# Optimization experiments

Hardware: AMD Instinct MI355X
Metric: run time of the kernel (lower is better)

The kernel has to match this reference:

```python
import jax, jax.numpy as jnp
import numpy as np

BN_EPS = 1e-5

def setup_inputs() -> dict:
    key = jax.random.key(0)
    ks = jax.random.split(key, 13)
    bs, ch, hei, wei = 4, 32, 32, 128  # n_features = wei = 128, ch = n_features//4
    nf = wei
    def p(k, shape, s=0.05):
        return jax.random.normal(k, shape, dtype=jnp.float32) * s
    return {
        "head": jax.random.normal(ks[0], (bs, ch, hei, wei), dtype=jnp.float32),
        "tail": jax.random.normal(ks[1], (bs, ch, hei, wei), dtype=jnp.float32),
        "R_q": p(ks[2], (nf, nf)), "R_k": p(ks[3], (nf, nf)),
        "R_v": p(ks[4], (nf, nf)), "R_W": p(ks[5], (nf, nf)),
        "F_q": p(ks[6], (nf, nf)), "F_k": p(ks[7], (nf, nf)),
        "F_v": p(ks[8], (nf, nf)), "F_W": p(ks[9], (nf, nf)),
        "conv_w": p(ks[10], (2, 2 * ch, 1, 1)),
        "conv_b": jnp.zeros((2,), jnp.float32),
        "bn_w": jnp.ones((2,), jnp.float32),
        "bn_b": jnp.zeros((2,), jnp.float32),
        "bn_mean": jnp.zeros((2,), jnp.float32),
        "bn_var": jnp.ones((2,), jnp.float32),
        "flag": 1,
    }

def _affinity(head, tail, conv_w, conv_b, bn_w, bn_b, bn_mean, bn_var):
    # 1x1 conv -> eval-mode BatchNorm2d -> ReLU -> softmax over channel dim
    x = jnp.concatenate([head, tail], axis=1)                       # [b,2c,h,w]
    a = jnp.einsum('bchw,oc->bohw', x, conv_w[:, :, 0, 0]) + conv_b[None, :, None, None]
    scale = (bn_w / jnp.sqrt(bn_var + BN_EPS))[None, :, None, None]
    a = (a - bn_mean[None, :, None, None]) * scale + bn_b[None, :, None, None]
    a = jax.nn.relu(a)
    return jax.nn.softmax(a, axis=1)                                # torch legacy dim=1 for 4D

def reference(head, tail, R_q, R_k, R_v, R_W, F_q, F_k, F_v, F_W,
              conv_w, conv_b, bn_w, bn_b, bn_mean, bn_var, flag):
    bs, ch, hei, wei = head.shape
    L = hei * wei
    ic = ch  # inter_channels == ch by construction
    aff = _affinity(head, tail, conv_w, conv_b, bn_w, bn_b, bn_mean, bn_var)
    if flag:
        alpha = aff[:, 0].reshape(bs, L, 1)                          # broadcast over last axis
        q = (head @ R_q).reshape(bs, ic, L).transpose(0, 2, 1)       # [b,L,ic]
        t_k = (tail @ F_k).reshape(bs, ic, L).transpose(0, 2, 1)     # [b,L,ic]
        t_v = (tail @ F_v).reshape(bs, ic, L)                        # [b,ic,L]
        f_t = t_k @ t_v                                              # [b,L,L]
        h_k = (head @ R_k).reshape(bs, ic, L).transpose(0, 2, 1)
        h_v = (head @ R_v).reshape(bs, ic, L)
        f_h = h_k @ h_v                                              # [b,L,L]
        att = jax.nn.softmax(alpha * f_t + f_h, axis=-1)
        y = (att @ q).transpose(0, 2, 1).reshape(bs, ic, hei, wei)
        return y @ R_W + head
    else:
        alpha = aff[:, 1].reshape(bs, L, 1)
        q = (tail @ F_q).reshape(bs, ic, L).transpose(0, 2, 1)
        h_k = (head @ R_k).reshape(bs, ic, L).transpose(0, 2, 1)
        h_v = (head @ R_v).reshape(bs, ic, L)
        f_h = h_k @ h_v
        t_k = (tail @ F_k).reshape(bs, ic, L).transpose(0, 2, 1)
        t_v = (tail @ F_v).reshape(bs, ic, L)
        f_t = t_k @ t_v
        att = jax.nn.softmax(alpha * f_h + f_t, axis=-1)
        y = (att @ q).transpose(0, 2, 1).reshape(bs, ic, hei, wei)
        return y @ F_W + tail
```

## Files before the change

kernel.cpp:

```cpp
#include <hip/hip_runtime.h>
#include <hip/hip_bf16.h>
#include <stdint.h>

typedef unsigned short u16;
typedef unsigned int u32;
typedef __attribute__((ext_vector_type(8))) short short8;
typedef __attribute__((ext_vector_type(4))) short short4_t;
typedef __attribute__((ext_vector_type(4))) float f32x4;

#define MFMA16(A,B,C) __builtin_amdgcn_mfma_f32_16x16x32_bf16((A),(B),(C),0,0,0)
#define L2E 1.4426950408889634f

__device__ __forceinline__ u16 f2bf(float f) {
  u32 x = __float_as_uint(f);
  u32 r = x + 0x7fffu + ((x >> 16) & 1u);
  return (u16)(r >> 16);
}
__device__ __forceinline__ float bf2f(short v) {
  return __uint_as_float((u32)(u16)v << 16);
}
__device__ __forceinline__ u32 pack_bf2(float a, float b) {
  __hip_bfloat162 h = __float22bfloat162_rn(make_float2(a, b));
  u32 u; __builtin_memcpy(&u, &h, 4); return u;
}
__device__ __forceinline__ short8 mk_frag(u32 w0, u32 w1, u32 w2, u32 w3) {
  union { u32 u[4]; short8 s; } cv;
  cv.u[0] = w0; cv.u[1] = w1; cv.u[2] = w2; cv.u[3] = w3;
  return cv.s;
}
__device__ __forceinline__ float vmax4(f32x4 v) {
  return fmaxf(fmaxf(v[0], v[1]), fmaxf(v[2], v[3]));
}
__device__ __forceinline__ float vsum4(f32x4 v) {
  return (v[0] + v[1]) + (v[2] + v[3]);
}

#if __has_builtin(__builtin_amdgcn_permlane16_swap) && __has_builtin(__builtin_amdgcn_permlane32_swap)
__device__ __forceinline__ float quad_max16(float x) {
  u32 xu = __float_as_uint(x);
  auto a = __builtin_amdgcn_permlane16_swap(xu, xu, false, false);
  float m = fmaxf(__uint_as_float(a[0]), __uint_as_float(a[1]));
  u32 mu = __float_as_uint(m);
  auto b = __builtin_amdgcn_permlane32_swap(mu, mu, false, false);
  return fmaxf(__uint_as_float(b[0]), __uint_as_float(b[1]));
}
__device__ __forceinline__ float quad_sum16(float x) {
  u32 xu = __float_as_uint(x);
  auto a = __builtin_amdgcn_permlane16_swap(xu, xu, false, false);
  float m = __uint_as_float(a[0]) + __uint_as_float(a[1]);
  u32 mu = __float_as_uint(m);
  auto b = __builtin_amdgcn_permlane32_swap(mu, mu, false, false);
  return __uint_as_float(b[0]) + __uint_as_float(b[1]);
}
#else
__device__ __forceinline__ float quad_max16(float x) {
  x = fmaxf(x, __shfl_xor(x, 16, 64));
  return fmaxf(x, __shfl_xor(x, 32, 64));
}
__device__ __forceinline__ float quad_sum16(float x) {
  x += __shfl_xor(x, 16, 64);
  return x + __shfl_xor(x, 32, 64);
}
#endif

__global__ void kprep(const float* R_q, const float* R_k, const float* R_v,
                      const float* R_W, const float* F_q, const float* F_k,
                      const float* F_v, const float* F_W, const int* flagp,
                      u16* matT)
{
  int flag = *flagp;
  const float* S;
  int m = blockIdx.x;
  if (flag) {
    const float* s[6] = {R_q, R_k, R_v, F_k, F_v, R_W}; S = s[m];
  } else {
    const float* s[6] = {F_q, F_k, F_v, R_k, R_v, F_W}; S = s[m];
  }
  u16* dst = matT + m * 16384;
  int base = blockIdx.y * 2048;
  for (int idx = base + threadIdx.x; idx < base + 2048; idx += blockDim.x) {
    int k = idx >> 7, n = idx & 127;
    dst[n * 128 + k] = f2bf(S[idx]);
  }
}

__global__ __launch_bounds__(256) void kproj(const float* __restrict__ head,
    const float* __restrict__ tail, const u16* __restrict__ matT,
    const float* __restrict__ conv_w, const float* __restrict__ conv_b,
    const float* __restrict__ bn_w, const float* __restrict__ bn_b,
    const float* __restrict__ bn_mean, const float* __restrict__ bn_var,
    u16* __restrict__ qT, u16* __restrict__ KQ,
    u16* __restrict__ Vc, const int* __restrict__ flagp)
{
  __shared__ u16 lds_t[128][34];
  __shared__ float s_alpha[128];
  const int flag = *flagp;
  const float* X1 = flag ? head : tail;
  const float* X2 = flag ? tail : head;
  const int bh = blockIdx.x, g = blockIdx.y;
  const int b = bh >> 5, h = bh & 31;
  const float* src = (g < 3) ? X1 : X2;
  const u16* Bm = matT + g * 16384;
  const int tid = threadIdx.x, lane = tid & 63, wid = tid >> 6;
  const int lrow = lane & 15, lg = lane >> 4;
  const int rt = wid & 1, cbase = (wid >> 1) * 64;

  if (g == 3) {
    if (tid < 128) {
      int w = tid;
      const float* hp = head + ((size_t)b * 1024 + h) * 128 + w;
      const float* tp = tail + ((size_t)b * 1024 + h) * 128 + w;
      float a0 = 0.f, a1 = 0.f;
      for (int c = 0; c < 32; ++c) {
        float xh = hp[c * 4096];
        float xt = tp[c * 4096];
        a0 += xh * conv_w[c]      + xt * conv_w[32 + c];
        a1 += xh * conv_w[64 + c] + xt * conv_w[96 + c];
      }
      const float eps = 1e-5f;
      a0 += conv_b[0]; a1 += conv_b[1];
      a0 = (a0 - bn_mean[0]) * (bn_w[0] * rsqrtf(bn_var[0] + eps)) + bn_b[0];
      a1 = (a1 - bn_mean[1]) * (bn_w[1] * rsqrtf(bn_var[1] + eps)) + bn_b[1];
      a0 = fmaxf(a0, 0.f); a1 = fmaxf(a1, 0.f);
      float asel = flag ? a0 : a1, aoth = flag ? a1 : a0;
      s_alpha[w] = 1.f / (1.f + __expf(aoth - asel));
    }
    __syncthreads();
  }

  f32x4 acc[4] = {};
  const float* Arow = src + (((size_t)b * 32 + rt * 16 + lrow) * 32 + h) * 128;
  #pragma unroll
  for (int k0 = 0; k0 < 128; k0 += 32) {
    const float* ap = Arow + k0 + lg * 8;
    float4 f0 = *reinterpret_cast<const float4*>(ap);
    float4 f1 = *reinterpret_cast<const float4*>(ap + 4);
    short8 af = mk_frag(pack_bf2(f0.x, f0.y), pack_bf2(f0.z, f0.w),
                        pack_bf2(f1.x, f1.y), pack_bf2(f1.z, f1.w));
    #pragma unroll
    for (int cc = 0; cc < 4; ++cc) {
      short8 bf = *reinterpret_cast<const short8*>(
          Bm + (cbase + cc * 16 + lrow) * 128 + k0 + lg * 8);
      acc[cc] = MFMA16(af, bf, acc[cc]);
    }
  }
  #pragma unroll
  for (int cc = 0; cc < 4; ++cc) {
    int n = cbase + cc * 16 + lrow;
    float asc = (g == 1) ? L2E : 1.f;
    if (g == 3) asc = s_alpha[n] * L2E;
    #pragma unroll
    for (int rr = 0; rr < 4; ++rr) {
      int c = rt * 16 + lg * 4 + rr;
      lds_t[n][c] = f2bf(acc[cc][rr] * asc);
    }
  }
  __syncthreads();
  if (g == 0) {
    int c = tid >> 3, w0 = (tid & 7) * 16;
    int tw[8];
    #pragma unroll
    for (int i2 = 0; i2 < 8; ++i2)
      tw[i2] = (int)lds_t[w0 + 2 * i2][c] | ((int)lds_t[w0 + 2 * i2 + 1][c] << 16);
    int4* dst = reinterpret_cast<int4*>(qT + ((size_t)b * 32 + c) * 4096 + h * 128 + w0);
    dst[0] = make_int4(tw[0], tw[1], tw[2], tw[3]);
    dst[1] = make_int4(tw[4], tw[5], tw[6], tw[7]);
  } else if (tid < 128) {
    int w = tid;
    int tw[16];
    #pragma unroll
    for (int i2 = 0; i2 < 16; ++i2)
      tw[i2] = (int)lds_t[w][2 * i2] | ((int)lds_t[w][2 * i2 + 1] << 16);
    u16* base = (g == 2 || g == 4) ? Vc : KQ;
    int coff = (g >= 3) ? 32 : 0;
    int4* dst = reinterpret_cast<int4*>(base + ((size_t)b * 4096 + h * 128 + w) * 64 + coff);
    dst[0] = make_int4(tw[0],  tw[1],  tw[2],  tw[3]);
    dst[1] = make_int4(tw[4],  tw[5],  tw[6],  tw[7]);
    dst[2] = make_int4(tw[8],  tw[9],  tw[10], tw[11]);
    dst[3] = make_int4(tw[12], tw[13], tw[14], tw[15]);
  }
}

__global__ __launch_bounds__(256, 6) void kattn(const u16* __restrict__ qT,
    const u16* __restrict__ KQ, const u16* __restrict__ Vc,
    u16* __restrict__ pO, float* __restrict__ pm, float* __restrict__ pl)
{
  __shared__ __align__(16) char lds_v[2][8192];
  __shared__ __align__(16) char lds_q[2][4096];
  const int b = blockIdx.y;
  const int i0 = blockIdx.x * 64;
  const int sp = blockIdx.z;
  const int jbase = sp * 512;
  const int tid = threadIdx.x, lane = tid & 63, wid = tid >> 6;
  const int lrow = lane & 15, lg = lane >> 4;

  const u16* KQb = KQ + (size_t)b * 4096 * 64;
  const u16* Vb  = Vc + (size_t)b * 4096 * 64;
  const u16* qTb = qT + (size_t)b * 32 * 4096;

  short8 bkq[2];
  {
    int r = i0 + wid * 16 + lrow;
    #pragma unroll
    for (int kc = 0; kc < 2; ++kc)
      bkq[kc] = *reinterpret_cast<const short8*>(KQb + (size_t)r * 64 + kc * 32 + lg * 8);
  }

  const int sr = tid >> 3, sx = (tid & 7) * 16;
  const int pr = (((sr >> 2) & 3) << 3) + (((sr >> 4) & 1) << 2) + (sr & 3);

  #pragma unroll
  for (int q = 0; q < 2; ++q) {
    int r = sr + q * 32, gr = pr + q * 32;
    int4 v = *reinterpret_cast<const int4*>(
        reinterpret_cast<const char*>(Vb + (size_t)(jbase + gr) * 64) + sx);
    *reinterpret_cast<int4*>(lds_v[0] + r * 128 + (sx ^ ((r & 7) << 4))) = v;
  }
  {
    int4 qv = *reinterpret_cast<const int4*>(
        qTb + (size_t)sr * 4096 + jbase + (tid & 7) * 8);
    *reinterpret_cast<int4*>(lds_q[0] + sr * 128 + (sx ^ ((sr & 7) << 4))) = qv;
  }
  __syncthreads();

  float m_run = -1e30f, l_run = 0.f;
  f32x4 accO[2] = {};
  int4 stgV[2], stgQ;

  for (int t = 0; t < 8; ++t) {
    const int buf = t & 1;
    if (t < 7) {
      const u16* Vn = Vb + (size_t)(jbase + (t + 1) * 64) * 64;
      #pragma unroll
      for (int q = 0; q < 2; ++q) {
        int gr = pr + q * 32;
        stgV[q] = *reinterpret_cast<const int4*>(
            reinterpret_cast<const char*>(Vn + (size_t)gr * 64) + sx);
      }
      stgQ = *reinterpret_cast<const int4*>(
          qTb + (size_t)sr * 4096 + jbase + (t + 1) * 64 + (tid & 7) * 8);
    }
    f32x4 st[4];
    __builtin_amdgcn_s_setprio(1);
    #pragma unroll
    for (int sub = 0; sub < 4; ++sub) {
      f32x4 a = {};
      #pragma unroll
      for (int kc = 0; kc < 2; ++kc) {
        int r = sub * 16 + lrow;
        int xs = kc * 64 + lg * 16;
        short8 av = *reinterpret_cast<const short8*>(
            lds_v[buf] + r * 128 + (xs ^ ((r & 7) << 4)));
        a = MFMA16(av, bkq[kc], a);
      }
      st[sub] = a;
    }
    __builtin_amdgcn_s_setprio(0);
    short8 aq[2][2];
    #pragma unroll
    for (int w = 0; w < 2; ++w)
      #pragma unroll
      for (int ct = 0; ct < 2; ++ct) {
        int r = ct * 16 + lrow;
        int xs = w * 64 + lg * 16;
        aq[w][ct] = *reinterpret_cast<const short8*>(
            lds_q[buf] + r * 128 + (xs ^ ((r & 7) << 4)));
      }
    float tm = fmaxf(fmaxf(vmax4(st[0]), vmax4(st[1])),
                     fmaxf(vmax4(st[2]), vmax4(st[3])));
    tm = quad_max16(tm);
    if (!__all((int)(tm <= m_run + 8.f))) {
      float m_new = fmaxf(m_run, tm);
      float scale = exp2f(m_run - m_new);
      l_run *= scale;
      #pragma unroll
      for (int ct = 0; ct < 2; ++ct)
        #pragma unroll
        for (int rr = 0; rr < 4; ++rr) accO[ct][rr] *= scale;
      m_run = m_new;
    }
    #pragma unroll
    for (int sub = 0; sub < 4; ++sub)
      #pragma unroll
      for (int rr = 0; rr < 4; ++rr)
        st[sub][rr] = exp2f(st[sub][rr] - m_run);
    float ps = (vsum4(st[0]) + vsum4(st[1])) + (vsum4(st[2]) + vsum4(st[3]));
    l_run += quad_sum16(ps);

    __builtin_amdgcn_s_setprio(1);
    #pragma unroll
    for (int w = 0; w < 2; ++w) {
      short8 bp = mk_frag(pack_bf2(st[2 * w][0],     st[2 * w][1]),
                          pack_bf2(st[2 * w][2],     st[2 * w][3]),
                          pack_bf2(st[2 * w + 1][0], st[2 * w + 1][1]),
                          pack_bf2(st[2 * w + 1][2], st[2 * w + 1][3]));
      #pragma unroll
      for (int ct = 0; ct < 2; ++ct)
        accO[ct] = MFMA16(aq[w][ct], bp, accO[ct]);
    }
    __builtin_amdgcn_s_setprio(0);

    if (t < 7) {
      #pragma unroll
      for (int q = 0; q < 2; ++q) {
        int r = sr + q * 32;
        *reinterpret_cast<int4*>(lds_v[buf ^ 1] + r * 128 + (sx ^ ((r & 7) << 4))) = stgV[q];
      }
      *reinterpret_cast<int4*>(lds_q[buf ^ 1] + sr * 128 + (sx ^ ((sr & 7) << 4))) = stgQ;
      __syncthreads();
    }
  }

  const int i = i0 + wid * 16 + lrow;
  u16* pOb = pO + (size_t)((b * 8 + sp) * 32) * 4096;
  #pragma unroll
  for (int ct = 0; ct < 2; ++ct)
    #pragma unroll
    for (int rr = 0; rr < 4; ++rr)
      pOb[(size_t)(ct * 16 + lg * 4 + rr) * 4096 + i] = f2bf(accO[ct][rr]);
  if (lg == 0) {
    pm[(b * 8 + sp) * 4096 + i] = m_run;
    pl[(b * 8 + sp) * 4096 + i] = l_run;
  }
}

__global__ __launch_bounds__(256) void kout(const u16* __restrict__ pO,
    const float* __restrict__ pm, const float* __restrict__ pl,
    const u16* __restrict__ matT, const float* __restrict__ head,
    const float* __restrict__ tail, const int* __restrict__ flagp,
    float* __restrict__ out)
{
  __shared__ u16 ylds[32][136];
  const int flag = *flagp;
  const float* X1 = flag ? head : tail;
  const u16* Bm = matT + 5 * 16384;
  const int tid = threadIdx.x;
  const int b = blockIdx.x >> 5, c = blockIdx.x & 31;
  const int rbase = blockIdx.x * 32;
  const int ioff = tid * 16;

  #pragma unroll
  for (int iq = 0; iq < 4; ++iq) {
    float4 msp[8];
    #pragma unroll
    for (int sp = 0; sp < 8; ++sp)
      msp[sp] = *reinterpret_cast<const float4*>(
          pm + (size_t)((b * 8 + sp) * 4096) + ioff + iq * 4);
    float4 M4 = msp[0];
    #pragma unroll
    for (int sp = 1; sp < 8; ++sp) {
      M4.x = fmaxf(M4.x, msp[sp].x); M4.y = fmaxf(M4.y, msp[sp].y);
      M4.z = fmaxf(M4.z, msp[sp].z); M4.w = fmaxf(M4.w, msp[sp].w);
    }
    float4 L4 = {0.f, 0.f, 0.f, 0.f}, y4 = {0.f, 0.f, 0.f, 0.f};
    #pragma unroll
    for (int sp = 0; sp < 8; ++sp) {
      float4 w4;
      w4.x = exp2f(msp[sp].x - M4.x); w4.y = exp2f(msp[sp].y - M4.y);
      w4.z = exp2f(msp[sp].z - M4.z); w4.w = exp2f(msp[sp].w - M4.w);
      float4 l4 = *reinterpret_cast<const float4*>(
          pl + (size_t)((b * 8 + sp) * 4096) + ioff + iq * 4);
      L4.x += w4.x * l4.x; L4.y += w4.y * l4.y;
      L4.z += w4.z * l4.z; L4.w += w4.w * l4.w;
      short4_t o4 = *reinterpret_cast<const short4_t*>(
          pO + (size_t)(((b * 8 + sp) * 32 + c)) * 4096 + ioff + iq * 4);
      y4.x += w4.x * bf2f(o4[0]); y4.y += w4.y * bf2f(o4[1]);
      y4.z += w4.z * bf2f(o4[2]); y4.w += w4.w * bf2f(o4[3]);
    }
    y4.x /= L4.x; y4.y /= L4.y; y4.z /= L4.z; y4.w /= L4.w;
    uint2 pk2;
    pk2.x = pack_bf2(y4.x, y4.y);
    pk2.y = pack_bf2(y4.z, y4.w);
    *reinterpret_cast<uint2*>(&ylds[tid >> 3][(tid & 7) * 16 + iq * 4]) = pk2;
  }
  __syncthreads();

  const int lane = tid & 63, wid = tid >> 6;
  const int lrow = lane & 15, lg = lane >> 4;
  const int rg = (wid & 1) * 16, cg = (wid >> 1) * 64;
  f32x4 acc[4] = {};
  #pragma unroll
  for (int k0 = 0; k0 < 128; k0 += 32) {
    short8 af = *reinterpret_cast<const short8*>(&ylds[rg + lrow][k0 + lg * 8]);
    #pragma unroll
    for (int cc = 0; cc < 4; ++cc) {
      short8 bf = *reinterpret_cast<const short8*>(
          Bm + (size_t)(cg + cc * 16 + lrow) * 128 + k0 + lg * 8);
      acc[cc] = MFMA16(af, bf, acc[cc]);
    }
  }
  #pragma unroll
  for (int cc = 0; cc < 4; ++cc)
    #pragma unroll
    for (int rr = 0; rr < 4; ++rr) {
      int row = rbase + rg + lg * 4 + rr;
      int col = cg + cc * 16 + lrow;
      size_t idx = (size_t)row * 128 + col;
      out[idx] = acc[cc][rr] + X1[idx];
    }
}

extern "C" void kernel_launch(void* const* d_in, const int* in_sizes, int n_in,
                              void* d_out, int out_size, void* d_ws, size_t ws_size,
                              hipStream_t stream)
{
  const float* head    = (const float*)d_in[0];
  const float* tail    = (const float*)d_in[1];
  const float* R_q     = (const float*)d_in[2];
  const float* R_k     = (const float*)d_in[3];
  const float* R_v     = (const float*)d_in[4];
  const float* R_W     = (const float*)d_in[5];
  const float* F_q     = (const float*)d_in[6];
  const float* F_k     = (const float*)d_in[7];
  const float* F_v     = (const float*)d_in[8];
  const float* F_W     = (const float*)d_in[9];
  const float* conv_w  = (const float*)d_in[10];
  const float* conv_b  = (const float*)d_in[11];
  const float* bn_w    = (const float*)d_in[12];
  const float* bn_b    = (const float*)d_in[13];
  const float* bn_mean = (const float*)d_in[14];
  const float* bn_var  = (const float*)d_in[15];
  const int*   flagp   = (const int*)d_in[16];
  float* out = (float*)d_out;

  char* ws = (char*)d_ws;
  u16*   matT = (u16*)(ws);
  u16*   qT   = (u16*)(ws + 262144);
  u16*   KQ   = (u16*)(ws + 1310720);
  u16*   Vc   = (u16*)(ws + 3407872);
  u16*   pO   = (u16*)(ws + 6553600);
  float* pm   = (float*)(ws + 14942208);
  float* pl   = (float*)(ws + 15466496);

  kprep <<<dim3(6, 8), 256, 0, stream>>>(R_q, R_k, R_v, R_W, F_q, F_k, F_v, F_W, flagp, matT);
  kproj <<<dim3(128, 5), 256, 0, stream>>>(head, tail, matT, conv_w, conv_b,
                                           bn_w, bn_b, bn_mean, bn_var,
                                           qT, KQ, Vc, flagp);
  kattn <<<dim3(64, 4, 8), 256, 0, stream>>>(qT, KQ, Vc, pO, pm, pl);
  kout  <<<128, 256, 0, stream>>>(pO, pm, pl, matT, head, tail, flagp, out);
}
```

Baseline: 66.28 us.

## Double split-K count in attention, preload all tiles, add separate merge kernel

```diff
diff --git a/kernel.cpp b/kernel.cpp
--- a/kernel.cpp
+++ b/kernel.cpp
@@ -181,16 +181,16 @@
   }
 }
 
-__global__ __launch_bounds__(256, 6) void kattn(const u16* __restrict__ qT,
+__global__ __launch_bounds__(256, 3) void kattn(const u16* __restrict__ qT,
     const u16* __restrict__ KQ, const u16* __restrict__ Vc,
     u16* __restrict__ pO, float* __restrict__ pm, float* __restrict__ pl)
 {
-  __shared__ __align__(16) char lds_v[2][8192];
-  __shared__ __align__(16) char lds_q[2][4096];
+  __shared__ __align__(16) char lds_v[4][8192];
+  __shared__ __align__(16) char lds_q[4][4096];
   const int b = blockIdx.y;
   const int i0 = blockIdx.x * 64;
   const int sp = blockIdx.z;
-  const int jbase = sp * 512;
+  const int jbase = sp * 256;
   const int tid = threadIdx.x, lane = tid & 63, wid = tid >> 6;
   const int lrow = lane & 15, lg = lane >> 4;
 
@@ -208,38 +208,26 @@
 
   const int sr = tid >> 3, sx = (tid & 7) * 16;
   const int pr = (((sr >> 2) & 3) << 3) + (((sr >> 4) & 1) << 2) + (sr & 3);
-
-  #pragma unroll
-  for (int q = 0; q < 2; ++q) {
-    int r = sr + q * 32, gr = pr + q * 32;
-    int4 v = *reinterpret_cast<const int4*>(
-        reinterpret_cast<const char*>(Vb + (size_t)(jbase + gr) * 64) + sx);
-    *reinterpret_cast<int4*>(lds_v[0] + r * 128 + (sx ^ ((r & 7) << 4))) = v;
-  }
-  {
+  #pragma unroll
+  for (int t = 0; t < 4; ++t) {
+    #pragma unroll
+    for (int q = 0; q < 2; ++q) {
+      int r = sr + q * 32, gr = pr + q * 32;
+      int4 v = *reinterpret_cast<const int4*>(
+          reinterpret_cast<const char*>(Vb + (size_t)(jbase + t * 64 + gr) * 64) + sx);
+      *reinterpret_cast<int4*>(lds_v[t] + r * 128 + (sx ^ ((r & 7) << 4))) = v;
+    }
     int4 qv = *reinterpret_cast<const int4*>(
-        qTb + (size_t)sr * 4096 + jbase + (tid & 7) * 8);
-    *reinterpret_cast<int4*>(lds_q[0] + sr * 128 + (sx ^ ((sr & 7) << 4))) = qv;
+        qTb + (size_t)sr * 4096 + jbase + t * 64 + (tid & 7) * 8);
+    *reinterpret_cast<int4*>(lds_q[t] + sr * 128 + (sx ^ ((sr & 7) << 4))) = qv;
   }
   __syncthreads();
 
   float m_run = -1e30f, l_run = 0.f;
   f32x4 accO[2] = {};
-  int4 stgV[2], stgQ;
-
-  for (int t = 0; t < 8; ++t) {
-    const int buf = t & 1;
-    if (t < 7) {
-      const u16* Vn = Vb + (size_t)(jbase + (t + 1) * 64) * 64;
-      #pragma unroll
-      for (int q = 0; q < 2; ++q) {
-        int gr = pr + q * 32;
-        stgV[q] = *reinterpret_cast<const int4*>(
-            reinterpret_cast<const char*>(Vn + (size_t)gr * 64) + sx);
-      }
-      stgQ = *reinterpret_cast<const int4*>(
-          qTb + (size_t)sr * 4096 + jbase + (t + 1) * 64 + (tid & 7) * 8);
-    }
+
+  #pragma unroll
+  for (int t = 0; t < 4; ++t) {
     f32x4 st[4];
     __builtin_amdgcn_s_setprio(1);
     #pragma unroll
@@ -250,7 +238,7 @@
         int r = sub * 16 + lrow;
         int xs = kc * 64 + lg * 16;
         short8 av = *reinterpret_cast<const short8*>(
-            lds_v[buf] + r * 128 + (xs ^ ((r & 7) << 4)));
+            lds_v[t] + r * 128 + (xs ^ ((r & 7) << 4)));
         a = MFMA16(av, bkq[kc], a);
       }
       st[sub] = a;
@@ -264,7 +252,7 @@
         int r = ct * 16 + lrow;
         int xs = w * 64 + lg * 16;
         aq[w][ct] = *reinterpret_cast<const short8*>(
-            lds_q[buf] + r * 128 + (xs ^ ((r & 7) << 4)));
+            lds_q[t] + r * 128 + (xs ^ ((r & 7) << 4)));
       }
     float tm = fmaxf(fmaxf(vmax4(st[0]), vmax4(st[1])),
                      fmaxf(vmax4(st[2]), vmax4(st[3])));
@@ -299,36 +287,48 @@
         accO[ct] = MFMA16(aq[w][ct], bp, accO[ct]);
     }
     __builtin_amdgcn_s_setprio(0);
-
-    if (t < 7) {
-      #pragma unroll
-      for (int q = 0; q < 2; ++q) {
-        int r = sr + q * 32;
-        *reinterpret_cast<int4*>(lds_v[buf ^ 1] + r * 128 + (sx ^ ((r & 7) << 4))) = stgV[q];
-      }
-      *reinterpret_cast<int4*>(lds_q[buf ^ 1] + sr * 128 + (sx ^ ((sr & 7) << 4))) = stgQ;
-      __syncthreads();
-    }
   }
 
   const int i = i0 + wid * 16 + lrow;
-  u16* pOb = pO + (size_t)((b * 8 + sp) * 32) * 4096;
+  u16* pOb = pO + (size_t)((b * 16 + sp) * 32) * 4096;
   #pragma unroll
   for (int ct = 0; ct < 2; ++ct)
     #pragma unroll
     for (int rr = 0; rr < 4; ++rr)
       pOb[(size_t)(ct * 16 + lg * 4 + rr) * 4096 + i] = f2bf(accO[ct][rr]);
   if (lg == 0) {
-    pm[(b * 8 + sp) * 4096 + i] = m_run;
-    pl[(b * 8 + sp) * 4096 + i] = l_run;
-  }
+    pm[(b * 16 + sp) * 4096 + i] = m_run;
+    pl[(b * 16 + sp) * 4096 + i] = l_run;
+  }
+}
+
+__global__ __launch_bounds__(256) void kmerge(const float* __restrict__ pm,
+    const float* __restrict__ pl, float* __restrict__ wm)
+{
+  const int b = blockIdx.y;
+  const int i = blockIdx.x * 256 + threadIdx.x;
+  float m[16], M = -1e30f;
+  #pragma unroll
+  for (int sp = 0; sp < 16; ++sp) {
+    m[sp] = pm[(b * 16 + sp) * 4096 + i];
+    M = fmaxf(M, m[sp]);
+  }
+  float L = 0.f;
+  #pragma unroll
+  for (int sp = 0; sp < 16; ++sp) {
+    m[sp] = exp2f(m[sp] - M);
+    L += m[sp] * pl[(b * 16 + sp) * 4096 + i];
+  }
+  float inv = 1.f / L;
+  #pragma unroll
+  for (int sp = 0; sp < 16; ++sp)
+    wm[(b * 16 + sp) * 4096 + i] = m[sp] * inv;
 }
 
 __global__ __launch_bounds__(256) void kout(const u16* __restrict__ pO,
-    const float* __restrict__ pm, const float* __restrict__ pl,
-    const u16* __restrict__ matT, const float* __restrict__ head,
-    const float* __restrict__ tail, const int* __restrict__ flagp,
-    float* __restrict__ out)
+    const float* __restrict__ wm, const u16* __restrict__ matT,
+    const float* __restrict__ head, const float* __restrict__ tail,
+    const int* __restrict__ flagp, float* __restrict__ out)
 {
   __shared__ u16 ylds[32][136];
   const int flag = *flagp;
@@ -341,33 +341,16 @@
 
   #pragma unroll
   for (int iq = 0; iq < 4; ++iq) {
-    float4 msp[8];
-    #pragma unroll
-    for (int sp = 0; sp < 8; ++sp)
-      msp[sp] = *reinterpret_cast<const float4*>(
-          pm + (size_t)((b * 8 + sp) * 4096) + ioff + iq * 4);
-    float4 M4 = msp[0];
-    #pragma unroll
-    for (int sp = 1; sp < 8; ++sp) {
-      M4.x = fmaxf(M4.x, msp[sp].x); M4.y = fmaxf(M4.y, msp[sp].y);
-      M4.z = fmaxf(M4.z, msp[sp].z); M4.w = fmaxf(M4.w, msp[sp].w);
-    }
-    float4 L4 = {0.f, 0.f, 0.f, 0.f}, y4 = {0.f, 0.f, 0.f, 0.f};
-    #pragma unroll
-    for (int sp = 0; sp < 8; ++sp) {
-      float4 w4;
-      w4.x = exp2f(msp[sp].x - M4.x); w4.y = exp2f(msp[sp].y - M4.y);
-      w4.z = exp2f(msp[sp].z - M4.z); w4.w = exp2f(msp[sp].w - M4.w);
-      float4 l4 = *reinterpret_cast<const float4*>(
-          pl + (size_t)((b * 8 + sp) * 4096) + ioff + iq * 4);
-      L4.x += w4.x * l4.x; L4.y += w4.y * l4.y;
-      L4.z += w4.z * l4.z; L4.w += w4.w * l4.w;
+    float4 y4 = {0.f, 0.f, 0.f, 0.f};
+    #pragma unroll
+    for (int sp = 0; sp < 16; ++sp) {
+      float4 w4 = *reinterpret_cast<const float4*>(
+          wm + (size_t)((b * 16 + sp) * 4096) + ioff + iq * 4);
       short4_t o4 = *reinterpret_cast<const short4_t*>(
-          pO + (size_t)(((b * 8 + sp) * 32 + c)) * 4096 + ioff + iq * 4);
+          pO + (size_t)(((b * 16 + sp) * 32 + c)) * 4096 + ioff + iq * 4);
       y4.x += w4.x * bf2f(o4[0]); y4.y += w4.y * bf2f(o4[1]);
       y4.z += w4.z * bf2f(o4[2]); y4.w += w4.w * bf2f(o4[3]);
     }
-    y4.x /= L4.x; y4.y /= L4.y; y4.z /= L4.z; y4.w /= L4.w;
     uint2 pk2;
     pk2.x = pack_bf2(y4.x, y4.y);
     pk2.y = pack_bf2(y4.z, y4.w);
@@ -429,13 +412,15 @@
   u16*   KQ   = (u16*)(ws + 1310720);
   u16*   Vc   = (u16*)(ws + 3407872);
   u16*   pO   = (u16*)(ws + 6553600);
-  float* pm   = (float*)(ws + 14942208);
-  float* pl   = (float*)(ws + 15466496);
+  float* pm   = (float*)(ws + 23330816);
+  float* pl   = (float*)(ws + 24379392);
+  float* wm   = (float*)(ws + 25427968);
 
   kprep <<<dim3(6, 8), 256, 0, stream>>>(R_q, R_k, R_v, R_W, F_q, F_k, F_v, F_W, flagp, matT);
   kproj <<<dim3(128, 5), 256, 0, stream>>>(head, tail, matT, conv_w, conv_b,
                                            bn_w, bn_b, bn_mean, bn_var,
                                            qT, KQ, Vc, flagp);
-  kattn <<<dim3(64, 4, 8), 256, 0, stream>>>(qT, KQ, Vc, pO, pm, pl);
-  kout  <<<128, 256, 0, stream>>>(pO, pm, pl, matT, head, tail, flagp, out);
-}
+  kattn <<<dim3(64, 4, 16), 256, 0, stream>>>(qT, KQ, Vc, pO, pm, pl);
+  kmerge<<<dim3(16, 4), 256, 0, stream>>>(pm, pl, wm);
+  kout  <<<128, 256, 0, stream>>>(pO, wm, matT, head, tail, flagp, out);
+}
```

Result: slower. 69.56 us (+4.9%).

## Switch attention kernel to 32x32 MFMA tiles with 128-row query blocks

Applied to the files above, without the earlier changes.

```diff
diff --git a/kernel.cpp b/kernel.cpp
--- a/kernel.cpp
+++ b/kernel.cpp
@@ -7,8 +7,10 @@
 typedef __attribute__((ext_vector_type(8))) short short8;
 typedef __attribute__((ext_vector_type(4))) short short4_t;
 typedef __attribute__((ext_vector_type(4))) float f32x4;
+typedef __attribute__((ext_vector_type(16))) float f32x16;
 
 #define MFMA16(A,B,C) __builtin_amdgcn_mfma_f32_16x16x32_bf16((A),(B),(C),0,0,0)
+#define MFMA32(A,B,C) __builtin_amdgcn_mfma_f32_32x32x16_bf16((A),(B),(C),0,0,0)
 #define L2E 1.4426950408889634f
 
 __device__ __forceinline__ u16 f2bf(float f) {
@@ -28,37 +30,23 @@
   cv.u[0] = w0; cv.u[1] = w1; cv.u[2] = w2; cv.u[3] = w3;
   return cv.s;
 }
-__device__ __forceinline__ float vmax4(f32x4 v) {
-  return fmaxf(fmaxf(v[0], v[1]), fmaxf(v[2], v[3]));
-}
-__device__ __forceinline__ float vsum4(f32x4 v) {
-  return (v[0] + v[1]) + (v[2] + v[3]);
-}
-
-#if __has_builtin(__builtin_amdgcn_permlane16_swap) && __has_builtin(__builtin_amdgcn_permlane32_swap)
-__device__ __forceinline__ float quad_max16(float x) {
+
+#if __has_builtin(__builtin_amdgcn_permlane32_swap)
+__device__ __forceinline__ float half_max(float x) {
   u32 xu = __float_as_uint(x);
-  auto a = __builtin_amdgcn_permlane16_swap(xu, xu, false, false);
-  float m = fmaxf(__uint_as_float(a[0]), __uint_as_float(a[1]));
-  u32 mu = __float_as_uint(m);
-  auto b = __builtin_amdgcn_permlane32_swap(mu, mu, false, false);
-  return fmaxf(__uint_as_float(b[0]), __uint_as_float(b[1]));
-}
-__device__ __forceinline__ float quad_sum16(float x) {
+  auto a = __builtin_amdgcn_permlane32_swap(xu, xu, false, false);
+  return fmaxf(__uint_as_float(a[0]), __uint_as_float(a[1]));
+}
+__device__ __forceinline__ float half_sum(float x) {
   u32 xu = __float_as_uint(x);
-  auto a = __builtin_amdgcn_permlane16_swap(xu, xu, false, false);
-  float m = __uint_as_float(a[0]) + __uint_as_float(a[1]);
-  u32 mu = __float_as_uint(m);
-  auto b = __builtin_amdgcn_permlane32_swap(mu, mu, false, false);
-  return __uint_as_float(b[0]) + __uint_as_float(b[1]);
+  auto a = __builtin_amdgcn_permlane32_swap(xu, xu, false, false);
+  return __uint_as_float(a[0]) + __uint_as_float(a[1]);
 }
 #else
-__device__ __forceinline__ float quad_max16(float x) {
-  x = fmaxf(x, __shfl_xor(x, 16, 64));
+__device__ __forceinline__ float half_max(float x) {
   return fmaxf(x, __shfl_xor(x, 32, 64));
 }
-__device__ __forceinline__ float quad_sum16(float x) {
-  x += __shfl_xor(x, 16, 64);
+__device__ __forceinline__ float half_sum(float x) {
   return x + __shfl_xor(x, 32, 64);
 }
 #endif
@@ -181,37 +169,36 @@
   }
 }
 
-__global__ __launch_bounds__(256, 6) void kattn(const u16* __restrict__ qT,
+__global__ __launch_bounds__(256, 4) void kattn(const u16* __restrict__ qT,
     const u16* __restrict__ KQ, const u16* __restrict__ Vc,
     u16* __restrict__ pO, float* __restrict__ pm, float* __restrict__ pl)
 {
   __shared__ __align__(16) char lds_v[2][8192];
   __shared__ __align__(16) char lds_q[2][4096];
   const int b = blockIdx.y;
-  const int i0 = blockIdx.x * 64;
+  const int i0 = blockIdx.x * 128;
   const int sp = blockIdx.z;
   const int jbase = sp * 512;
   const int tid = threadIdx.x, lane = tid & 63, wid = tid >> 6;
-  const int lrow = lane & 15, lg = lane >> 4;
+  const int l31 = lane & 31, h = lane >> 5;
+  const int iw = i0 + wid * 32;
 
   const u16* KQb = KQ + (size_t)b * 4096 * 64;
   const u16* Vb  = Vc + (size_t)b * 4096 * 64;
   const u16* qTb = qT + (size_t)b * 32 * 4096;
 
-  short8 bkq[2];
-  {
-    int r = i0 + wid * 16 + lrow;
-    #pragma unroll
-    for (int kc = 0; kc < 2; ++kc)
-      bkq[kc] = *reinterpret_cast<const short8*>(KQb + (size_t)r * 64 + kc * 32 + lg * 8);
-  }
+  short8 bkq[4];
+  #pragma unroll
+  for (int c = 0; c < 4; ++c)
+    bkq[c] = *reinterpret_cast<const short8*>(
+        KQb + (size_t)(iw + l31) * 64 + c * 16 + h * 8);
 
   const int sr = tid >> 3, sx = (tid & 7) * 16;
-  const int pr = (((sr >> 2) & 3) << 3) + (((sr >> 4) & 1) << 2) + (sr & 3);
+  const int pr0 = (sr & ~12) | ((sr & 4) << 1) | ((sr & 8) >> 1);
 
   #pragma unroll
   for (int q = 0; q < 2; ++q) {
-    int r = sr + q * 32, gr = pr + q * 32;
+    int r = sr + q * 32, gr = pr0 + q * 32;
     int4 v = *reinterpret_cast<const int4*>(
         reinterpret_cast<const char*>(Vb + (size_t)(jbase + gr) * 64) + sx);
     *reinterpret_cast<int4*>(lds_v[0] + r * 128 + (sx ^ ((r & 7) << 4))) = v;
@@ -224,7 +211,7 @@
   __syncthreads();
 
   float m_run = -1e30f, l_run = 0.f;
-  f32x4 accO[2] = {};
+  f32x16 accO = {};
   int4 stgV[2], stgQ;
 
   for (int t = 0; t < 8; ++t) {
@@ -233,70 +220,66 @@
       const u16* Vn = Vb + (size_t)(jbase + (t + 1) * 64) * 64;
       #pragma unroll
       for (int q = 0; q < 2; ++q) {
-        int gr = pr + q * 32;
+        int gr = pr0 + q * 32;
         stgV[q] = *reinterpret_cast<const int4*>(
             reinterpret_cast<const char*>(Vn + (size_t)gr * 64) + sx);
       }
       stgQ = *reinterpret_cast<const int4*>(
           qTb + (size_t)sr * 4096 + jbase + (t + 1) * 64 + (tid & 7) * 8);
     }
-    f32x4 st[4];
+    f32x16 st[2];
+    st[0] = f32x16{}; st[1] = f32x16{};
     __builtin_amdgcn_s_setprio(1);
     #pragma unroll
-    for (int sub = 0; sub < 4; ++sub) {
-      f32x4 a = {};
-      #pragma unroll
-      for (int kc = 0; kc < 2; ++kc) {
-        int r = sub * 16 + lrow;
-        int xs = kc * 64 + lg * 16;
+    for (int jt = 0; jt < 2; ++jt) {
+      int vr = jt * 32 + l31;
+      #pragma unroll
+      for (int c = 0; c < 4; ++c) {
         short8 av = *reinterpret_cast<const short8*>(
-            lds_v[buf] + r * 128 + (xs ^ ((r & 7) << 4)));
-        a = MFMA16(av, bkq[kc], a);
+            lds_v[buf] + vr * 128 + ((c * 32 + h * 16) ^ ((vr & 7) << 4)));
+        st[jt] = MFMA32(av, bkq[c], st[jt]);
       }
-      st[sub] = a;
     }
     __builtin_amdgcn_s_setprio(0);
-    short8 aq[2][2];
-    #pragma unroll
-    for (int w = 0; w < 2; ++w)
-      #pragma unroll
-      for (int ct = 0; ct < 2; ++ct) {
-        int r = ct * 16 + lrow;
-        int xs = w * 64 + lg * 16;
-        aq[w][ct] = *reinterpret_cast<const short8*>(
-            lds_q[buf] + r * 128 + (xs ^ ((r & 7) << 4)));
-      }
-    float tm = fmaxf(fmaxf(vmax4(st[0]), vmax4(st[1])),
-                     fmaxf(vmax4(st[2]), vmax4(st[3])));
-    tm = quad_max16(tm);
+    short8 aq[4];
+    #pragma unroll
+    for (int cc = 0; cc < 4; ++cc)
+      aq[cc] = *reinterpret_cast<const short8*>(
+          lds_q[buf] + l31 * 128 + ((cc * 32 + h * 16) ^ ((l31 & 7) << 4)));
+    float tm = -1e30f;
+    #pragma unroll
+    for (int jt = 0; jt < 2; ++jt)
+      #pragma unroll
+      for (int r = 0; r < 16; ++r) tm = fmaxf(tm, st[jt][r]);
+    tm = half_max(tm);
     if (!__all((int)(tm <= m_run + 8.f))) {
       float m_new = fmaxf(m_run, tm);
       float scale = exp2f(m_run - m_new);
       l_run *= scale;
       #pragma unroll
-      for (int ct = 0; ct < 2; ++ct)
-        #pragma unroll
-        for (int rr = 0; rr < 4; ++rr) accO[ct][rr] *= scale;
+      for (int r = 0; r < 16; ++r) accO[r] *= scale;
       m_run = m_new;
     }
-    #pragma unroll
-    for (int sub = 0; sub < 4; ++sub)
-      #pragma unroll
-      for (int rr = 0; rr < 4; ++rr)
-        st[sub][rr] = exp2f(st[sub][rr] - m_run);
-    float ps = (vsum4(st[0]) + vsum4(st[1])) + (vsum4(st[2]) + vsum4(st[3]));
-    l_run += quad_sum16(ps);
+    float ps = 0.f;
+    #pragma unroll
+    for (int jt = 0; jt < 2; ++jt)
+      #pragma unroll
+      for (int r = 0; r < 16; ++r) {
+        float p = exp2f(st[jt][r] - m_run);
+        st[jt][r] = p;
+        ps += p;
+      }
+    l_run += half_sum(ps);
 
     __builtin_amdgcn_s_setprio(1);
     #pragma unroll
-    for (int w = 0; w < 2; ++w) {
-      short8 bp = mk_frag(pack_bf2(st[2 * w][0],     st[2 * w][1]),
-                          pack_bf2(st[2 * w][2],     st[2 * w][3]),
-                          pack_bf2(st[2 * w + 1][0], st[2 * w + 1][1]),
-                          pack_bf2(st[2 * w + 1][2], st[2 * w + 1][3]));
-      #pragma unroll
-      for (int ct = 0; ct < 2; ++ct)
-        accO[ct] = MFMA16(aq[w][ct], bp, accO[ct]);
+    for (int cc = 0; cc < 4; ++cc) {
+      const int jt = cc >> 1, p8 = (cc & 1) * 8;
+      short8 bp = mk_frag(pack_bf2(st[jt][p8 + 0], st[jt][p8 + 1]),
+                          pack_bf2(st[jt][p8 + 2], st[jt][p8 + 3]),
+                          pack_bf2(st[jt][p8 + 4], st[jt][p8 + 5]),
+                          pack_bf2(st[jt][p8 + 6], st[jt][p8 + 7]));
+      accO = MFMA32(aq[cc], bp, accO);
     }
     __builtin_amdgcn_s_setprio(0);
 
@@ -311,14 +294,14 @@
     }
   }
 
-  const int i = i0 + wid * 16 + lrow;
+  const int i = iw + l31;
   u16* pOb = pO + (size_t)((b * 8 + sp) * 32) * 4096;
   #pragma unroll
-  for (int ct = 0; ct < 2; ++ct)
-    #pragma unroll
-    for (int rr = 0; rr < 4; ++rr)
-      pOb[(size_t)(ct * 16 + lg * 4 + rr) * 4096 + i] = f2bf(accO[ct][rr]);
-  if (lg == 0) {
+  for (int r = 0; r < 16; ++r) {
+    int c = (r & 3) + 8 * (r >> 2) + 4 * h;
+    pOb[(size_t)c * 4096 + i] = f2bf(accO[r]);
+  }
+  if (h == 0) {
     pm[(b * 8 + sp) * 4096 + i] = m_run;
     pl[(b * 8 + sp) * 4096 + i] = l_run;
   }
@@ -436,6 +419,6 @@
   kproj <<<dim3(128, 5), 256, 0, stream>>>(head, tail, matT, conv_w, conv_b,
                                            bn_w, bn_b, bn_mean, bn_var,
                                            qT, KQ, Vc, flagp);
-  kattn <<<dim3(64, 4, 8), 256, 0, stream>>>(qT, KQ, Vc, pO, pm, pl);
+  kattn <<<dim3(32, 4, 8), 256, 0, stream>>>(qT, KQ, Vc, pO, pm, pl);
   kout  <<<128, 256, 0, stream>>>(pO, pm, pl, matT, head, tail, flagp, out);
 }
```

After: 64.12 us. -3.3%, faster.
